# Performance work log

Hardware: AMD Instinct MI355X
Metric: run time of the kernel (lower is better)

## Reference

```python
import jax, jax.numpy as jnp
import numpy as np

NEG_INF = -9e15


def setup_inputs() -> dict:
    key = jax.random.key(0)
    k1, k2, k3, k4, k5 = jax.random.split(key, 5)
    N, F_IN, F_OUT = 8192, 512, 256
    x = jax.random.normal(k1, (N, F_IN), dtype=jnp.float32)
    adjacent_matrix = jax.random.randint(k2, (N, N), 0, 2, dtype=jnp.int32)
    # xavier-normal-like scales (gain sqrt(2))
    W = jax.random.normal(k3, (F_IN, F_OUT), dtype=jnp.float32) * np.sqrt(2.0) * np.sqrt(2.0 / (F_IN + F_OUT))
    a1 = jax.random.normal(k4, (F_OUT, 1), dtype=jnp.float32) * np.sqrt(2.0) * np.sqrt(2.0 / (F_OUT + 1))
    a2 = jax.random.normal(k5, (F_OUT, 1), dtype=jnp.float32) * np.sqrt(2.0) * np.sqrt(2.0 / (F_OUT + 1))
    return {"x": x, "adjacent_matrix": adjacent_matrix, "W": W, "a1": a1, "a2": a2}


def reference(x, adjacent_matrix, W, a1, a2):
    alpha = 0.2  # LeakyReLU negative slope
    h = x @ W                                   # [N, F_out]
    f1 = h @ a1                                 # [N, 1]
    f2 = h @ a2                                 # [N, 1]
    e = f1 + f2.T                               # [N, N] broadcast pairwise scores
    e = jnp.where(e > 0, e, alpha * e)          # LeakyReLU
    e = jnp.where(adjacent_matrix > 0, e, NEG_INF)  # mask non-edges
    attention = jax.nn.softmax(e, axis=1)       # [N, N]
    h_prime = attention @ h                     # [N, F_out]
    return jax.nn.elu(h_prime)                  # concat=True -> ELU
```

## Files before the change

kernel.cpp:

```cpp
#include <hip/hip_runtime.h>
#include <hip/hip_bf16.h>

#define N_NODES 8192
#define F_IN 512
#define F_OUT 256
#define KSPLIT 4
#define KCHUNK (N_NODES / KSPLIT)

using short8 = __attribute__((ext_vector_type(8))) short;
using f32x4  = __attribute__((ext_vector_type(4))) float;

__device__ __forceinline__ short f2bf(float v) {
    union { float f; unsigned u; } x; x.f = v;
    unsigned r = x.u + 0x7fffu + ((x.u >> 16) & 1u);
    return (short)(r >> 16);
}

__global__ void k_prep(const float* __restrict__ W, const float* __restrict__ a1,
                       const float* __restrict__ a2, float* __restrict__ w1,
                       float* __restrict__ w2, short* __restrict__ WTg) {
    const int k = blockIdx.x;
    const int l = threadIdx.x;
    float4 wv = *(const float4*)(W + (size_t)k * F_OUT + 4 * l);
    float4 av = *(const float4*)(a1 + 4 * l);
    float4 bv = *(const float4*)(a2 + 4 * l);
    float s1 = wv.x*av.x + wv.y*av.y + wv.z*av.z + wv.w*av.w;
    float s2 = wv.x*bv.x + wv.y*bv.y + wv.z*bv.z + wv.w*bv.w;
    WTg[(size_t)(4*l+0)*F_IN + k] = f2bf(wv.x);
    WTg[(size_t)(4*l+1)*F_IN + k] = f2bf(wv.y);
    WTg[(size_t)(4*l+2)*F_IN + k] = f2bf(wv.z);
    WTg[(size_t)(4*l+3)*F_IN + k] = f2bf(wv.w);
    #pragma unroll
    for (int off = 32; off; off >>= 1) {
        s1 += __shfl_down(s1, off);
        s2 += __shfl_down(s2, off);
    }
    if (l == 0) { w1[k] = s1; w2[k] = s2; }
}

__global__ void k_f12(const float* __restrict__ x, const float* __restrict__ w1,
                      const float* __restrict__ w2, float* __restrict__ f1,
                      float* __restrict__ f2) {
    const int wv = threadIdx.x >> 6, l = threadIdx.x & 63;
    const int i = blockIdx.x * 4 + wv;
    const float* xr = x + (size_t)i * F_IN;
    float s1 = 0.f, s2 = 0.f;
    #pragma unroll
    for (int t = 0; t < 2; ++t) {
        int k = t * 256 + l * 4;
        float4 xv = *(const float4*)(xr + k);
        float4 u  = *(const float4*)(w1 + k);
        float4 v  = *(const float4*)(w2 + k);
        s1 += xv.x*u.x + xv.y*u.y + xv.z*u.z + xv.w*u.w;
        s2 += xv.x*v.x + xv.y*v.y + xv.z*v.z + xv.w*v.w;
    }
    #pragma unroll
    for (int off = 32; off; off >>= 1) {
        s1 += __shfl_down(s1, off);
        s2 += __shfl_down(s2, off);
    }
    if (l == 0) { f1[i] = s1; f2[i] = s2; }
}

__launch_bounds__(256)
__global__ void k_hT(const float* __restrict__ x, const short* __restrict__ WTg,
                     short* __restrict__ hT) {
    __shared__ short x_lds[32 * 64];
    __shared__ short wt_lds[256 * 64];
    const int tid = threadIdx.x;
    const int wv = tid >> 6, l = tid & 63, lg = l >> 4, lr = l & 15;
    const int ibase = blockIdx.x * 32;
    f32x4 acc[4][2];
    #pragma unroll
    for (int a = 0; a < 4; ++a)
        #pragma unroll
        for (int b = 0; b < 2; ++b) acc[a][b] = (f32x4){0.f, 0.f, 0.f, 0.f};
    for (int k0 = 0; k0 < F_IN; k0 += 64) {
        __syncthreads();
        {
            int i = tid >> 3, ch = tid & 7;
            const float* src = x + (size_t)(ibase + i) * F_IN + k0 + ch * 8;
            float4 v0 = *(const float4*)(src);
            float4 v1 = *(const float4*)(src + 4);
            short8 s;
            s[0]=f2bf(v0.x); s[1]=f2bf(v0.y); s[2]=f2bf(v0.z); s[3]=f2bf(v0.w);
            s[4]=f2bf(v1.x); s[5]=f2bf(v1.y); s[6]=f2bf(v1.z); s[7]=f2bf(v1.w);
            *(short8*)&x_lds[i * 64 + 8 * (ch ^ (i & 7))] = s;
        }
        {
            int cb = tid >> 3, ch = tid & 7;
            #pragma unroll
            for (int p = 0; p < 8; ++p) {
                int c = cb + 32 * p;
                short8 s = *(const short8*)(WTg + (size_t)c * F_IN + k0 + ch * 8);
                *(short8*)&wt_lds[c * 64 + 8 * (ch ^ (c & 7))] = s;
            }
        }
        __syncthreads();
        #pragma unroll
        for (int ks = 0; ks < 2; ++ks) {
            short8 bfrag[2], afrag[4];
            #pragma unroll
            for (int it = 0; it < 2; ++it) {
                int i = it * 16 + lr;
                bfrag[it] = *(short8*)&x_lds[i * 64 + 8 * ((lg + 4*ks) ^ (i & 7))];
            }
            #pragma unroll
            for (int ct = 0; ct < 4; ++ct) {
                int c = wv * 64 + ct * 16 + lr;
                afrag[ct] = *(short8*)&wt_lds[c * 64 + 8 * ((lg + 4*ks) ^ (c & 7))];
            }
            #pragma unroll
            for (int ct = 0; ct < 4; ++ct)
                #pragma unroll
                for (int it = 0; it < 2; ++it)
                    acc[ct][it] = __builtin_amdgcn_mfma_f32_16x16x32_bf16(
                        afrag[ct], bfrag[it], acc[ct][it], 0, 0, 0);
        }
    }
    #pragma unroll
    for (int ct = 0; ct < 4; ++ct)
        #pragma unroll
        for (int it = 0; it < 2; ++it)
            #pragma unroll
            for (int r = 0; r < 4; ++r) {
                int c = wv * 64 + ct * 16 + 4 * lg + r;
                int i = ibase + it * 16 + lr;
                hT[(size_t)c * N_NODES + i] = f2bf(acc[ct][it][r]);
            }
}

__launch_bounds__(256, 2)
__global__ void k_attn(const int* __restrict__ adj, const short* __restrict__ hT,
                       const float* __restrict__ f1, const float* __restrict__ f2,
                       float* __restrict__ part, float* __restrict__ psum) {
    __shared__ short h_lds[256 * 64];
    __shared__ unsigned short am_lds[64 * 4];
    const int tid = threadIdx.x;
    const int wv = tid >> 6, l = tid & 63, lg = l >> 4, lr = l & 15;
    const int ksid = blockIdx.x >> 7;
    const int rowblk = blockIdx.x & 127;
    const int r0 = rowblk * 64;
    const int myrow = r0 + wv * 16 + lr;
    const int cb = tid >> 3, ch = tid & 7;
    const short* hsrc = hT + (size_t)cb * N_NODES + ch * 8;
    const int hswz = 8 * (ch ^ (cb & 7));
    const int q = l & 3, srow = wv * 16 + (l >> 2);
    const int* asrc = adj + (size_t)(r0 + srow) * N_NODES + q * 16;
    const int srow4 = srow * 4 + q;
    const int rowm4 = (wv * 16 + lr) * 4;
    const float f1v = f1[myrow];
    const float L2E = 1.44269504f;
    f32x4 acc[16];
    #pragma unroll
    for (int t = 0; t < 16; ++t) acc[t] = (f32x4){0.f, 0.f, 0.f, 0.f};
    float ps = 0.f;
    const int kbeg = ksid * KCHUNK;
    const int kend = kbeg + KCHUNK;

    short8 AH[8], BH[8];
    int4   AA[4], BA[4];

#define LOADT(K0, H, A) do {                                                   \
    _Pragma("unroll")                                                          \
    for (int p = 0; p < 8; ++p)                                                \
        H[p] = *(const short8*)(hsrc + (size_t)(32 * p) * N_NODES + (K0));     \
    _Pragma("unroll")                                                          \
    for (int p = 0; p < 4; ++p)                                                \
        A[p] = *(const int4*)(asrc + (K0) + p * 4);                            \
} while (0)

#define WRITET(H, A) do {                                                      \
    _Pragma("unroll")                                                          \
    for (int p = 0; p < 8; ++p)                                                \
        *(short8*)&h_lds[(cb + 32 * p) * 64 + hswz] = H[p];                    \
    unsigned m = 0;                                                            \
    _Pragma("unroll")                                                          \
    for (int p = 0; p < 4; ++p) {                                              \
        m |= (A[p].x > 0 ? 1u : 0u) << (4 * p);                                \
        m |= (A[p].y > 0 ? 2u : 0u) << (4 * p);                                \
        m |= (A[p].z > 0 ? 4u : 0u) << (4 * p);                                \
        m |= (A[p].w > 0 ? 8u : 0u) << (4 * p);                                \
    }                                                                          \
    am_lds[srow4] = (unsigned short)m;                                         \
} while (0)

#define COMPUTE(K0) do {                                                       \
    _Pragma("unroll")                                                          \
    for (int ks = 0; ks < 2; ++ks) {                                           \
        const int kg = (K0) + 32 * ks + 8 * lg;                                \
        const unsigned am = am_lds[rowm4 + 2 * ks + (lg >> 1)];                \
        const unsigned mbyte = (am >> (8 * (lg & 1))) & 0xffu;                 \
        const float4 fa = *(const float4*)(f2 + kg);                           \
        const float4 fb = *(const float4*)(f2 + kg + 4);                       \
        const float f2v[8] = {fa.x, fa.y, fa.z, fa.w, fb.x, fb.y, fb.z, fb.w}; \
        short8 pa;                                                             \
        _Pragma("unroll")                                                      \
        for (int j = 0; j < 8; ++j) {                                          \
            float ee = f1v + f2v[j];                                           \
            float le = fmaxf(ee, 0.2f * ee);                                   \
            float pv = (mbyte & (1u << j))                                     \
                           ? exp2f(fminf(le * L2E, 80.f)) : 0.f;               \
            ps += pv;                                                          \
            pa[j] = f2bf(pv);                                                  \
        }                                                                      \
        _Pragma("unroll")                                                      \
        for (int t = 0; t < 16; ++t) {                                         \
            const int c = t * 16 + lr;                                         \
            short8 bfrag = *(short8*)&h_lds[c * 64 + 8 * ((lg + 4*ks) ^ (lr & 7))]; \
            acc[t] = __builtin_amdgcn_mfma_f32_16x16x32_bf16(pa, bfrag, acc[t], 0, 0, 0); \
        }                                                                      \
    }                                                                          \
} while (0)

    LOADT(kbeg, AH, AA);
    for (int k0 = kbeg; k0 < kend; k0 += 128) {
        __syncthreads();
        WRITET(AH, AA);
        __syncthreads();
        LOADT(k0 + 64, BH, BA);
        COMPUTE(k0);
        __syncthreads();
        WRITET(BH, BA);
        __syncthreads();
        {
            const int kn = (k0 + 128 < kend) ? (k0 + 128) : kbeg;
            LOADT(kn, AH, AA);
        }
        COMPUTE(k0 + 64);
    }
#undef LOADT
#undef WRITET
#undef COMPUTE

    ps += __shfl_xor(ps, 16);
    ps += __shfl_xor(ps, 32);
    if (lg == 0) psum[ksid * N_NODES + myrow] = ps;
    float* pb = part + (size_t)ksid * N_NODES * F_OUT;
    #pragma unroll
    for (int t = 0; t < 16; ++t)
        #pragma unroll
        for (int r = 0; r < 4; ++r) {
            int row = r0 + wv * 16 + 4 * lg + r;
            int c = t * 16 + lr;
            pb[(size_t)row * F_OUT + c] = acc[t][r];
        }
}

__global__ void k_comb(const float* __restrict__ part, const float* __restrict__ psum,
                       float* __restrict__ out) {
    const int i = blockIdx.x, c = threadIdx.x;
    float o = 0.f, s = 0.f;
    #pragma unroll
    for (int qq = 0; qq < KSPLIT; ++qq) {
        o += part[(size_t)qq * N_NODES * F_OUT + (size_t)i * F_OUT + c];
        s += psum[qq * N_NODES + i];
    }
    float v = o / s;
    out[(size_t)i * F_OUT + c] = (v > 0.f) ? v : expm1f(v);
}

extern "C" void kernel_launch(void* const* d_in, const int* in_sizes, int n_in,
                              void* d_out, int out_size, void* d_ws, size_t ws_size,
                              hipStream_t stream) {
    const float* x  = (const float*)d_in[0];
    const int* adj  = (const int*)d_in[1];
    const float* W  = (const float*)d_in[2];
    const float* a1 = (const float*)d_in[3];
    const float* a2 = (const float*)d_in[4];
    float* out = (float*)d_out;

    short* hT  = (short*)d_ws;
    short* WTg = hT + (size_t)F_OUT * N_NODES;
    float* fb  = (float*)(WTg + (size_t)F_OUT * F_IN);
    float* w1   = fb;
    float* w2   = fb + 512;
    float* f1   = fb + 1024;
    float* f2   = fb + 1024 + N_NODES;
    float* part = fb + 32768;
    float* psum = part + (size_t)KSPLIT * N_NODES * F_OUT;

    k_prep<<<F_IN, 64, 0, stream>>>(W, a1, a2, w1, w2, WTg);
    k_f12<<<N_NODES / 4, 256, 0, stream>>>(x, w1, w2, f1, f2);
    k_hT<<<N_NODES / 32, 256, 0, stream>>>(x, WTg, hT);
    k_attn<<<128 * KSPLIT, 256, 0, stream>>>(adj, hT, f1, f2, part, psum);
    k_comb<<<N_NODES, 256, 0, stream>>>(part, psum, out);
}
```

Baseline: 477.8 us.

## Stage hT tiles via direct global-to-LDS loads with pre-swizzled layout and double buffer

k_hT now writes hT with an XOR swizzle baked into global memory. This lets k_attn use global_load_lds to copy tiles straight into a double-buffered LDS region with no register round trip or separate LDS write. The adjacency mask moves from LDS into registers and is shared between lanes with shuffles. MFMA sections get raised wave priority, and the block-to-split mapping is interleaved. These changes aim to cut register pressure, LDS store traffic and barriers per iteration, at the cost of twice the LDS footprint (64KB) for the double buffer.

New measurement: 448.9 us. -6.0%, faster.

```diff
diff --git a/kernel.cpp b/kernel.cpp
--- a/kernel.cpp
+++ b/kernel.cpp
@@ -9,6 +9,9 @@
 
 using short8 = __attribute__((ext_vector_type(8))) short;
 using f32x4  = __attribute__((ext_vector_type(4))) float;
+
+typedef __attribute__((address_space(3))) void lds_t;
+typedef const __attribute__((address_space(1))) void gbl_t;
 
 __device__ __forceinline__ short f2bf(float v) {
     union { float f; unsigned u; } x; x.f = v;
@@ -64,7 +67,7 @@
 
 __launch_bounds__(256)
 __global__ void k_hT(const float* __restrict__ x, const short* __restrict__ WTg,
-                     short* __restrict__ hT) {
+                     short* __restrict__ hTs) {
     __shared__ short x_lds[32 * 64];
     __shared__ short wt_lds[256 * 64];
     const int tid = threadIdx.x;
@@ -126,29 +129,25 @@
             for (int r = 0; r < 4; ++r) {
                 int c = wv * 64 + ct * 16 + 4 * lg + r;
                 int i = ibase + it * 16 + lr;
-                hT[(size_t)c * N_NODES + i] = f2bf(acc[ct][it][r]);
+                int isw = (i & ~56) | ((((i >> 3) & 7) ^ (c & 7)) << 3);
+                hTs[(size_t)c * N_NODES + isw] = f2bf(acc[ct][it][r]);
             }
 }
 
 __launch_bounds__(256, 2)
-__global__ void k_attn(const int* __restrict__ adj, const short* __restrict__ hT,
+__global__ void k_attn(const int* __restrict__ adj, const short* __restrict__ hTs,
                        const float* __restrict__ f1, const float* __restrict__ f2,
                        float* __restrict__ part, float* __restrict__ psum) {
-    __shared__ short h_lds[256 * 64];
-    __shared__ unsigned short am_lds[64 * 4];
+    __shared__ short h_lds[2 * 16384];
     const int tid = threadIdx.x;
     const int wv = tid >> 6, l = tid & 63, lg = l >> 4, lr = l & 15;
-    const int ksid = blockIdx.x >> 7;
-    const int rowblk = blockIdx.x & 127;
+    const int ksid = blockIdx.x & 3;
+    const int rowblk = blockIdx.x >> 2;
     const int r0 = rowblk * 64;
     const int myrow = r0 + wv * 16 + lr;
-    const int cb = tid >> 3, ch = tid & 7;
-    const short* hsrc = hT + (size_t)cb * N_NODES + ch * 8;
-    const int hswz = 8 * (ch ^ (cb & 7));
+    const short* hsrc = hTs + (size_t)(tid >> 3) * N_NODES + (tid & 7) * 8;
     const int q = l & 3, srow = wv * 16 + (l >> 2);
     const int* asrc = adj + (size_t)(r0 + srow) * N_NODES + q * 16;
-    const int srow4 = srow * 4 + q;
-    const int rowm4 = (wv * 16 + lr) * 4;
     const float f1v = f1[myrow];
     const float L2E = 1.44269504f;
     f32x4 acc[16];
@@ -158,80 +157,80 @@
     const int kbeg = ksid * KCHUNK;
     const int kend = kbeg + KCHUNK;
 
-    short8 AH[8], BH[8];
-    int4   AA[4], BA[4];
-
-#define LOADT(K0, H, A) do {                                                   \
-    _Pragma("unroll")                                                          \
-    for (int p = 0; p < 8; ++p)                                                \
-        H[p] = *(const short8*)(hsrc + (size_t)(32 * p) * N_NODES + (K0));     \
-    _Pragma("unroll")                                                          \
-    for (int p = 0; p < 4; ++p)                                                \
-        A[p] = *(const int4*)(asrc + (K0) + p * 4);                            \
-} while (0)
-
-#define WRITET(H, A) do {                                                      \
-    _Pragma("unroll")                                                          \
-    for (int p = 0; p < 8; ++p)                                                \
-        *(short8*)&h_lds[(cb + 32 * p) * 64 + hswz] = H[p];                    \
-    unsigned m = 0;                                                            \
-    _Pragma("unroll")                                                          \
-    for (int p = 0; p < 4; ++p) {                                              \
-        m |= (A[p].x > 0 ? 1u : 0u) << (4 * p);                                \
-        m |= (A[p].y > 0 ? 2u : 0u) << (4 * p);                                \
-        m |= (A[p].z > 0 ? 4u : 0u) << (4 * p);                                \
-        m |= (A[p].w > 0 ? 8u : 0u) << (4 * p);                                \
-    }                                                                          \
-    am_lds[srow4] = (unsigned short)m;                                         \
-} while (0)
-
-#define COMPUTE(K0) do {                                                       \
-    _Pragma("unroll")                                                          \
-    for (int ks = 0; ks < 2; ++ks) {                                           \
-        const int kg = (K0) + 32 * ks + 8 * lg;                                \
-        const unsigned am = am_lds[rowm4 + 2 * ks + (lg >> 1)];                \
-        const unsigned mbyte = (am >> (8 * (lg & 1))) & 0xffu;                 \
-        const float4 fa = *(const float4*)(f2 + kg);                           \
-        const float4 fb = *(const float4*)(f2 + kg + 4);                       \
-        const float f2v[8] = {fa.x, fa.y, fa.z, fa.w, fb.x, fb.y, fb.z, fb.w}; \
-        short8 pa;                                                             \
-        _Pragma("unroll")                                                      \
-        for (int j = 0; j < 8; ++j) {                                          \
-            float ee = f1v + f2v[j];                                           \
-            float le = fmaxf(ee, 0.2f * ee);                                   \
-            float pv = (mbyte & (1u << j))                                     \
-                           ? exp2f(fminf(le * L2E, 80.f)) : 0.f;               \
-            ps += pv;                                                          \
-            pa[j] = f2bf(pv);                                                  \
-        }                                                                      \
-        _Pragma("unroll")                                                      \
-        for (int t = 0; t < 16; ++t) {                                         \
-            const int c = t * 16 + lr;                                         \
-            short8 bfrag = *(short8*)&h_lds[c * 64 + 8 * ((lg + 4*ks) ^ (lr & 7))]; \
-            acc[t] = __builtin_amdgcn_mfma_f32_16x16x32_bf16(pa, bfrag, acc[t], 0, 0, 0); \
-        }                                                                      \
-    }                                                                          \
-} while (0)
-
-    LOADT(kbeg, AH, AA);
+    int4 AA[4], BA[4];
+
+#define STAGE(BUFOFF, K0) do {                                                  \
+    _Pragma("unroll")                                                           \
+    for (int p = 0; p < 8; ++p)                                                 \
+        __builtin_amdgcn_global_load_lds(                                       \
+            (gbl_t*)(hsrc + (size_t)p * 32 * N_NODES + (K0)),                   \
+            (lds_t*)&h_lds[(BUFOFF) + p * 2048 + wv * 512], 16, 0, 0);          \
+} while (0)
+
+#define ADJLOAD(A, K0) do {                                                     \
+    _Pragma("unroll")                                                           \
+    for (int p = 0; p < 4; ++p) A[p] = *(const int4*)(asrc + (K0) + p * 4);     \
+} while (0)
+
+#define COMPUTE_KS(K0, BUFOFF, AMV, KS) do {                                    \
+    const int kg = (K0) + 32 * (KS) + 8 * lg;                                   \
+    const unsigned mbyte = ((AMV) >> (8 * (lg & 1))) & 0xffu;                   \
+    const float4 fa = *(const float4*)(f2 + kg);                                \
+    const float4 fb4 = *(const float4*)(f2 + kg + 4);                           \
+    const float f2v[8] = {fa.x, fa.y, fa.z, fa.w, fb4.x, fb4.y, fb4.z, fb4.w};  \
+    short8 pa;                                                                  \
+    _Pragma("unroll")                                                           \
+    for (int j = 0; j < 8; ++j) {                                               \
+        float ee = f1v + f2v[j];                                                \
+        float le = fmaxf(ee, 0.2f * ee);                                        \
+        float pv = (mbyte & (1u << j)) ? exp2f(fminf(le * L2E, 80.f)) : 0.f;    \
+        ps += pv;                                                               \
+        pa[j] = f2bf(pv);                                                       \
+    }                                                                           \
+    const int swz = 8 * ((lg + 4 * (KS)) ^ (lr & 7));                           \
+    __builtin_amdgcn_s_setprio(1);                                              \
+    _Pragma("unroll")                                                           \
+    for (int t = 0; t < 16; ++t) {                                              \
+        short8 bfrag = *(short8*)&h_lds[(BUFOFF) + t * 1024 + lr * 64 + swz];   \
+        acc[t] = __builtin_amdgcn_mfma_f32_16x16x32_bf16(pa, bfrag, acc[t], 0, 0, 0); \
+    }                                                                           \
+    __builtin_amdgcn_s_setprio(0);                                              \
+} while (0)
+
+#define COMPUTE(K0, BUFOFF, A) do {                                             \
+    unsigned m = 0;                                                             \
+    _Pragma("unroll")                                                           \
+    for (int p = 0; p < 4; ++p) {                                               \
+        m |= (A[p].x > 0 ? 1u : 0u) << (4 * p);                                 \
+        m |= (A[p].y > 0 ? 2u : 0u) << (4 * p);                                 \
+        m |= (A[p].z > 0 ? 4u : 0u) << (4 * p);                                 \
+        m |= (A[p].w > 0 ? 8u : 0u) << (4 * p);                                 \
+    }                                                                           \
+    const unsigned am0 = (unsigned)__shfl((int)m, (lr << 2) | (lg >> 1));       \
+    const unsigned am1 = (unsigned)__shfl((int)m, (lr << 2) | 2 | (lg >> 1));   \
+    COMPUTE_KS(K0, BUFOFF, am0, 0);                                             \
+    COMPUTE_KS(K0, BUFOFF, am1, 1);                                             \
+} while (0)
+
+    STAGE(0, kbeg);
+    ADJLOAD(AA, kbeg);
+    __syncthreads();
     for (int k0 = kbeg; k0 < kend; k0 += 128) {
-        __syncthreads();
-        WRITET(AH, AA);
-        __syncthreads();
-        LOADT(k0 + 64, BH, BA);
-        COMPUTE(k0);
-        __syncthreads();
-        WRITET(BH, BA);
-        __syncthreads();
-        {
-            const int kn = (k0 + 128 < kend) ? (k0 + 128) : kbeg;
-            LOADT(kn, AH, AA);
-        }
-        COMPUTE(k0 + 64);
-    }
-#undef LOADT
-#undef WRITET
+        STAGE(16384, k0 + 64);
+        ADJLOAD(BA, k0 + 64);
+        COMPUTE(k0, 0, AA);
+        __syncthreads();
+        if (k0 + 128 < kend) {
+            STAGE(0, k0 + 128);
+            ADJLOAD(AA, k0 + 128);
+        }
+        COMPUTE(k0 + 64, 16384, BA);
+        __syncthreads();
+    }
+#undef STAGE
+#undef ADJLOAD
 #undef COMPUTE
+#undef COMPUTE_KS
 
     ps += __shfl_xor(ps, 16);
     ps += __shfl_xor(ps, 32);
@@ -270,8 +269,8 @@
     const float* a2 = (const float*)d_in[4];
     float* out = (float*)d_out;
 
-    short* hT  = (short*)d_ws;
-    short* WTg = hT + (size_t)F_OUT * N_NODES;
+    short* hTs = (short*)d_ws;
+    short* WTg = hTs + (size_t)F_OUT * N_NODES;
     float* fb  = (float*)(WTg + (size_t)F_OUT * F_IN);
     float* w1   = fb;
     float* w2   = fb + 512;
@@ -282,7 +281,7 @@
 
     k_prep<<<F_IN, 64, 0, stream>>>(W, a1, a2, w1, w2, WTg);
     k_f12<<<N_NODES / 4, 256, 0, stream>>>(x, w1, w2, f1, f2);
-    k_hT<<<N_NODES / 32, 256, 0, stream>>>(x, WTg, hT);
-    k_attn<<<128 * KSPLIT, 256, 0, stream>>>(adj, hT, f1, f2, part, psum);
+    k_hT<<<N_NODES / 32, 256, 0, stream>>>(x, WTg, hTs);
+    k_attn<<<128 * KSPLIT, 256, 0, stream>>>(adj, hTs, f1, f2, part, psum);
     k_comb<<<N_NODES, 256, 0, stream>>>(part, psum, out);
 }
```
